# Performance work log

Measured on AMD Instinct MI355X. Metric: run time of the kernel, lower is better.

Reference implementation:

```python
import jax, jax.numpy as jnp
import numpy as np

N = 100000      # nodes
E = 1600000     # edges
IN = 64         # in_channels
H = 64          # hidden_channels
OUT = 2         # out_channels
R = 8           # num_relations
B = 4           # num_bases
L = 3           # n_layers


def setup_inputs() -> dict:
    key = jax.random.key(0)
    ks = jax.random.split(key, 12)
    s = 0.1
    return {
        "x": jax.random.normal(ks[0], (N, IN), jnp.float32),
        "edge_index": jax.random.randint(ks[1], (2, E), 0, N, dtype=jnp.int64),
        "edge_type": jax.random.randint(ks[2], (E,), 0, R, dtype=jnp.int64),
        "lin1_w": jax.random.normal(ks[3], (IN, H), jnp.float32) * s,
        "lin1_b": jnp.zeros((H,), jnp.float32),
        # stacked per-layer RGCNConv params (basis decomposition)
        "bases": jax.random.normal(ks[4], (L, B, H, H), jnp.float32) * s,
        "comp": jax.random.normal(ks[5], (L, R, B), jnp.float32) * s,
        "root": jax.random.normal(ks[6], (L, H, H), jnp.float32) * s,
        "conv_bias": jnp.zeros((L, H), jnp.float32),
        "lin2_w": jax.random.normal(ks[7], (H, OUT), jnp.float32) * s,
        "lin2_b": jnp.zeros((OUT,), jnp.float32),
    }


def _rgcn_layer(h, src, dst, edge_type, bases, comp, root, bias):
    # basis decomposition: W_r = sum_b comp[r,b] * bases[b]  -> [R, H, H]
    W = jnp.einsum('rb,bio->rio', comp, bases)
    out = h @ root + bias  # root/self-loop term
    n = h.shape[0]
    for r in range(R):  # small fixed loop over relations
        hr = h @ W[r]                                  # [N, H] transform-then-gather
        mask = (edge_type == r)
        msg = jnp.where(mask[:, None], hr[src], jnp.zeros((), h.dtype))  # [E, H]
        ssum = jax.ops.segment_sum(msg, dst, num_segments=n)
        cnt = jax.ops.segment_sum(mask.astype(h.dtype), dst, num_segments=n)
        out = out + ssum / jnp.maximum(cnt, 1.0)[:, None]  # per-relation mean aggr
    return out


def reference(x, edge_index, edge_type, lin1_w, lin1_b, bases, comp, root,
              conv_bias, lin2_w, lin2_b):
    h = x @ lin1_w + lin1_b
    src, dst = edge_index[0], edge_index[1]
    for i in range(L):
        h_ = _rgcn_layer(h, src, dst, edge_type, bases[i], comp[i], root[i], conv_bias[i])
        if i < L - 1:
            # faithful to source: last conv output is discarded; dropout is
            # identity in eval mode
            h = h + jax.nn.relu(h_)
    return h @ lin2_w + lin2_b
```

## Files before the change

kernel.cpp:

```cpp
#include <hip/hip_runtime.h>


#define HDIM 64
#define RREL 8
#define NB   4
#define KC2  320
#define NPB  16
#define APAD 328

typedef short  short8 __attribute__((ext_vector_type(8)));
typedef __bf16 bf16x8 __attribute__((ext_vector_type(8)));
typedef float  f32x4  __attribute__((ext_vector_type(4)));
typedef unsigned int uint;
typedef unsigned short ushort;

static __device__ __forceinline__ ushort f2bf(float f) {
  uint u = __builtin_bit_cast(uint, f);
  u += 0x7FFFu + ((u >> 16) & 1u);
  return (ushort)(u >> 16);
}
static __device__ __forceinline__ float bf2f(ushort s) {
  uint u = ((uint)s) << 16;
  return __builtin_bit_cast(float, u);
}

__global__ void k_prep_wt(const float* __restrict__ lin1_w, const float* __restrict__ bases,
                          const float* __restrict__ root,
                          ushort* __restrict__ wt_lin1, ushort* __restrict__ wt_conv) {
  int t = blockIdx.x * 256 + threadIdx.x;
  if (t < HDIM * HDIM) {
    int j = t >> 6, k = t & 63;
    wt_lin1[t] = f2bf(lin1_w[k * HDIM + j]);
  }
  if (t < 2 * HDIM * KC2) {
    int l = t / (HDIM * KC2);
    int rem = t - l * (HDIM * KC2);
    int j = rem / KC2;
    int k = rem - j * KC2;
    float v;
    if (k < HDIM) {
      v = root[(l * HDIM + k) * HDIM + j];
    } else {
      int b = (k - HDIM) >> 6;
      int i = (k - HDIM) & 63;
      v = bases[((l * NB + b) * HDIM + i) * HDIM + j];
    }
    wt_conv[t] = f2bf(v);
  }
}

__global__ void k_chist(const int* __restrict__ dst, const int* __restrict__ et, int E,
                        uint* __restrict__ bcnt) {
  __shared__ uint cnt[1024];
  int t = threadIdx.x;
  for (int i = t; i < 1024; i += 256) cnt[i] = 0;
  __syncthreads();
  int per = (E + gridDim.x - 1) / gridDim.x;
  int e0 = blockIdx.x * per;
  int e1 = e0 + per; if (e1 > E) e1 = E;
  for (int e = e0 + t; e < e1; e += 256)
    atomicAdd(&cnt[((uint)dst[e] * RREL + (uint)et[e]) >> 10], 1u);
  __syncthreads();
  for (int i = t; i < 1024; i += 256)
    if (cnt[i]) atomicAdd(&bcnt[i], cnt[i]);
}

__global__ void k_scanB(const uint* __restrict__ bcnt, uint* __restrict__ boff,
                        uint* __restrict__ gcur, uint* __restrict__ off8,
                        int NBK, uint M8, uint E) {
  __shared__ uint s[1024];
  int t = threadIdx.x;
  uint v = (t < NBK) ? bcnt[t] : 0u;
  s[t] = v;
  __syncthreads();
  for (int o = 1; o < 1024; o <<= 1) {
    uint u = (t >= o) ? s[t - o] : 0u;
    __syncthreads();
    s[t] += u;
    __syncthreads();
  }
  uint ex = s[t] - v;
  if (t < NBK) { boff[t] = ex; gcur[t] = ex; }
  if (t == NBK - 1) boff[NBK] = s[t];
  if (t == 0) off8[M8] = E;
}

__global__ void k_cscat(const int* __restrict__ src, const int* __restrict__ dst,
                        const int* __restrict__ et, int E, uint* __restrict__ gcur,
                        uint* __restrict__ tmp) {
  __shared__ uint cnt[1024];
  __shared__ uint base[1024];
  int t = threadIdx.x;
  int per = (E + gridDim.x - 1) / gridDim.x;
  int e0 = blockIdx.x * per;
  int e1 = e0 + per; if (e1 > E) e1 = E;
  for (int i = t; i < 1024; i += 256) cnt[i] = 0;
  __syncthreads();
  for (int e = e0 + t; e < e1; e += 256) {
    uint key = (uint)dst[e] * RREL + (uint)et[e];
    atomicAdd(&cnt[key >> 10], 1u);
  }
  __syncthreads();
  for (int i = t; i < 1024; i += 256) {
    uint c = cnt[i];
    base[i] = c ? atomicAdd(&gcur[i], c) : 0u;
  }
  __syncthreads();
  for (int i = t; i < 1024; i += 256) cnt[i] = 0;
  __syncthreads();
  for (int e = e0 + t; e < e1; e += 256) {
    uint key = (uint)dst[e] * RREL + (uint)et[e];
    uint b = key >> 10;
    uint pos = base[b] + atomicAdd(&cnt[b], 1u);
    tmp[pos] = (uint)src[e] | ((key & 1023u) << 17);
  }
}

__global__ void k_fsort(const uint* __restrict__ boff, const uint* __restrict__ tmp,
                        uint* __restrict__ sorted, uint* __restrict__ off8, uint M8) {
  __shared__ uint c2[1024];
  __shared__ uint ex[1024];
  __shared__ uint s[256];
  int t = threadIdx.x;
  uint b = blockIdx.x;
  uint bo = boff[b], be = boff[b + 1];
  for (int i = t; i < 1024; i += 256) c2[i] = 0;
  __syncthreads();
  for (uint i = bo + t; i < be; i += 256) atomicAdd(&c2[tmp[i] >> 17], 1u);
  __syncthreads();
  int k4 = t * 4;
  uint v0 = c2[k4], v1 = c2[k4 + 1], v2 = c2[k4 + 2], v3 = c2[k4 + 3];
  uint tsum = v0 + v1 + v2 + v3;
  s[t] = tsum;
  __syncthreads();
  for (int o = 1; o < 256; o <<= 1) {
    uint u = (t >= o) ? s[t - o] : 0u;
    __syncthreads();
    s[t] += u;
    __syncthreads();
  }
  uint e0x = s[t] - tsum;
  ex[k4]     = e0x;
  ex[k4 + 1] = e0x + v0;
  ex[k4 + 2] = e0x + v0 + v1;
  ex[k4 + 3] = e0x + v0 + v1 + v2;
  __syncthreads();
  uint gbase = b << 10;
  #pragma unroll
  for (int u = 0; u < 4; ++u) {
    uint g = gbase + (uint)(k4 + u);
    if (g < M8) off8[g] = bo + ex[k4 + u];
  }
  for (int i = t; i < 1024; i += 256) c2[i] = 0;
  __syncthreads();
  for (uint i = bo + t; i < be; i += 256) {
    uint w = tmp[i];
    uint fk = w >> 17;
    uint pos = bo + ex[fk] + atomicAdd(&c2[fk], 1u);
    sorted[pos] = w & 0x1FFFFu;
  }
}

__global__ void k_lin1(const float* __restrict__ x, const ushort* __restrict__ wt,
                       const float* __restrict__ bias, ushort* __restrict__ hb, int N) {
  __shared__ ushort A[NPB][72];
  int nodebase = blockIdx.x * NPB;
  {
    int t = threadIdx.x;
    int nl = t >> 4, c = (t & 15) * 4;
    int n = nodebase + nl;
    ushort4 o = {0, 0, 0, 0};
    if (n < N) {
      f32x4 v = *(const f32x4*)&x[(size_t)n * HDIM + c];
      o.x = f2bf(v[0]); o.y = f2bf(v[1]); o.z = f2bf(v[2]); o.w = f2bf(v[3]);
    }
    *(ushort4*)&A[nl][c] = o;
  }
  __syncthreads();
  int lane = threadIdx.x & 63, wid = threadIdx.x >> 6;
  int m16 = lane & 15, khi = lane >> 4;
  int colbase = wid * 16;
  f32x4 acc = {0.f, 0.f, 0.f, 0.f};
  #pragma unroll
  for (int kk = 0; kk < HDIM; kk += 32) {
    int k0 = kk + khi * 8;
    short8 av = *(const short8*)&A[m16][k0];
    short8 bv = *(const short8*)&wt[(colbase + m16) * HDIM + k0];
    acc = __builtin_amdgcn_mfma_f32_16x16x32_bf16(
        __builtin_bit_cast(bf16x8, av), __builtin_bit_cast(bf16x8, bv), acc, 0, 0, 0);
  }
  int j = colbase + m16;
  float bj = bias[j];
  #pragma unroll
  for (int r = 0; r < 4; ++r) {
    int nl = khi * 4 + r;
    int n = nodebase + nl;
    if (n < N) hb[(size_t)n * HDIM + j] = f2bf(acc[r] + bj);
  }
}

__global__ void __launch_bounds__(256, 6)
k_conv(const uint* __restrict__ off8, const uint* __restrict__ sorted,
       const ushort* __restrict__ hb_in, const float* __restrict__ compL,
       const ushort* __restrict__ wt, const float* __restrict__ bias,
       ushort* __restrict__ hb_out, int N, int last,
       const float* __restrict__ w2, const float* __restrict__ b2,
       float* __restrict__ out) {
  __shared__ ushort A[NPB][APAD];
  __shared__ float  cmp[RREL * NB];
  __shared__ float  accO[NPB][2];
  int nb0 = blockIdx.x * NPB;
  int lane = threadIdx.x & 63, wid = threadIdx.x >> 6;

  if (threadIdx.x < RREL * NB) cmp[threadIdx.x] = compL[threadIdx.x];
  if (threadIdx.x < NPB * 2) accO[threadIdx.x >> 1][threadIdx.x & 1] = 0.f;
  {
    int t = threadIdx.x;
    int nl = t >> 4, c = (t & 15) * 4;
    int n = nb0 + nl;
    uint2 v = {0u, 0u};
    if (n < N) v = *(const uint2*)&hb_in[(size_t)n * HDIM + c];
    *(uint2*)&A[nl][c] = v;
  }
  __syncthreads();

  const ushort* hlane = hb_in + lane;
  for (int q = 0; q < 4; ++q) {
    int nl = wid * 4 + q;
    int n = nb0 + nl;
    if (n < N) {
      uint bv = 0xFFFFFFFFu;
      if (lane < 9) bv = off8[(uint)n * RREL + (uint)lane];
      uint s0 = (uint)__builtin_amdgcn_readlane((int)bv, 0);
      uint s1 = (uint)__builtin_amdgcn_readlane((int)bv, 8);
      float run = 0.f, z0 = 0.f, z1 = 0.f, z2 = 0.f, z3 = 0.f;
      int rel = 0;
      uint prevb = s0;
      uint nextb = (uint)__builtin_amdgcn_readlane((int)bv, 1);
      for (uint base = s0; base < s1; base += 16u) {
        const uint* sp = sorted + base;
        uint4 w0 = *(const uint4*)(sp);
        uint4 w1 = *(const uint4*)(sp + 4);
        uint4 w2v = *(const uint4*)(sp + 8);
        uint4 w3 = *(const uint4*)(sp + 12);
        uint idx[16] = {w0.x, w0.y, w0.z, w0.w, w1.x, w1.y, w1.z, w1.w,
                        w2v.x, w2v.y, w2v.z, w2v.w, w3.x, w3.y, w3.z, w3.w};
        float g[16];
        #pragma unroll
        for (int j = 0; j < 16; ++j) {
          uint ij = (uint)__builtin_amdgcn_readfirstlane((int)idx[j]) & 0x1FFFFu;
          g[j] = bf2f(hlane[(size_t)ij << 6]);
        }
        uint m = s1 - base;
        #pragma unroll
        for (int j = 0; j < 16; ++j) {
          if ((uint)j < m) {
            uint pos = base + (uint)j;
            while (pos >= nextb) {
              float mean = run * __builtin_amdgcn_rcpf(fmaxf((float)(nextb - prevb), 1.0f));
              f32x4 c4 = *(const f32x4*)&cmp[rel * NB];
              z0 += c4[0] * mean; z1 += c4[1] * mean;
              z2 += c4[2] * mean; z3 += c4[3] * mean;
              run = 0.f;
              ++rel;
              prevb = nextb;
              nextb = (uint)__builtin_amdgcn_readlane((int)bv, rel + 1);
            }
            run += g[j];
          }
        }
      }
      while (rel < RREL) {
        float mean = run * __builtin_amdgcn_rcpf(fmaxf((float)(nextb - prevb), 1.0f));
        f32x4 c4 = *(const f32x4*)&cmp[rel * NB];
        z0 += c4[0] * mean; z1 += c4[1] * mean;
        z2 += c4[2] * mean; z3 += c4[3] * mean;
        run = 0.f;
        ++rel;
        prevb = nextb;
        if (rel < RREL)
          nextb = (uint)__builtin_amdgcn_readlane((int)bv, rel + 1);
      }
      A[nl][HDIM + 0 * HDIM + lane] = f2bf(z0);
      A[nl][HDIM + 1 * HDIM + lane] = f2bf(z1);
      A[nl][HDIM + 2 * HDIM + lane] = f2bf(z2);
      A[nl][HDIM + 3 * HDIM + lane] = f2bf(z3);
    } else {
      #pragma unroll
      for (int b = 0; b < NB; ++b) A[nl][HDIM + b * HDIM + lane] = 0;
    }
  }
  __syncthreads();

  int m16 = lane & 15, khi = lane >> 4;
  int colbase = wid * 16;
  f32x4 acc = {0.f, 0.f, 0.f, 0.f};
  #pragma unroll
  for (int kk = 0; kk < KC2; kk += 32) {
    int k0 = kk + khi * 8;
    short8 av = *(const short8*)&A[m16][k0];
    short8 bv = *(const short8*)&wt[(uint)(colbase + m16) * KC2 + k0];
    acc = __builtin_amdgcn_mfma_f32_16x16x32_bf16(
        __builtin_bit_cast(bf16x8, av), __builtin_bit_cast(bf16x8, bv), acc, 0, 0, 0);
  }
  int j = colbase + m16;
  float bj = bias[j];
  if (!last) {
    #pragma unroll
    for (int r = 0; r < 4; ++r) {
      int nl = khi * 4 + r;
      int n = nb0 + nl;
      if (n < N) {
        float hs = bf2f(A[nl][j]);
        float hn = hs + fmaxf(acc[r] + bj, 0.f);
        hb_out[(uint)n * HDIM + j] = f2bf(hn);
      }
    }
  } else {
    float w0 = w2[j * 2], w1 = w2[j * 2 + 1];
    #pragma unroll
    for (int r = 0; r < 4; ++r) {
      int nl = khi * 4 + r;
      int n = nb0 + nl;
      float hn = 0.f;
      if (n < N) {
        float hs = bf2f(A[nl][j]);
        hn = hs + fmaxf(acc[r] + bj, 0.f);
      }
      float p0 = hn * w0, p1 = hn * w1;
      #pragma unroll
      for (int o = 1; o < 16; o <<= 1) {
        p0 += __shfl_xor(p0, o);
        p1 += __shfl_xor(p1, o);
      }
      if (m16 == 0 && n < N) {
        atomicAdd(&accO[nl][0], p0);
        atomicAdd(&accO[nl][1], p1);
      }
    }
    __syncthreads();
    if (threadIdx.x < NPB * 2) {
      int nl = threadIdx.x >> 1, o = threadIdx.x & 1;
      int n = nb0 + nl;
      if (n < N) out[2 * n + o] = accO[nl][o] + b2[o];
    }
  }
}

extern "C" void kernel_launch(void* const* d_in, const int* in_sizes, int n_in,
                              void* d_out, int out_size, void* d_ws, size_t ws_size,
                              hipStream_t stream) {
  const float* x      = (const float*)d_in[0];
  const int*   ei     = (const int*)d_in[1];
  const int*   et     = (const int*)d_in[2];
  const float* lin1_w = (const float*)d_in[3];
  const float* lin1_b = (const float*)d_in[4];
  const float* bases  = (const float*)d_in[5];
  const float* comp   = (const float*)d_in[6];
  const float* root   = (const float*)d_in[7];
  const float* cbias  = (const float*)d_in[8];
  const float* lin2_w = (const float*)d_in[9];
  const float* lin2_b = (const float*)d_in[10];
  float* out = (float*)d_out;

  int N = in_sizes[0] / HDIM;
  int E = in_sizes[2];
  uint M8 = (uint)N * RREL;
  int NBK = (int)((M8 + 1023u) >> 10);
  const int* srcp = ei;
  const int* dstp = ei + E;

  char* p = (char*)d_ws;
  auto carve = [&](size_t bytes) { char* r = p; p += (bytes + 255) & ~(size_t)255; return r; };
  ushort* hb_a    = (ushort*)carve((size_t)N * HDIM * 2);
  ushort* hb_b    = (ushort*)carve((size_t)N * HDIM * 2);
  uint*   sorted  = (uint*)carve((size_t)(E + 160) * 4);
  uint*   tmp     = (uint*)carve((size_t)E * 4);
  uint*   off8    = (uint*)carve((size_t)(M8 + 1) * 4);
  uint*   bcnt    = (uint*)carve(4096);
  uint*   boff    = (uint*)carve(4128);
  uint*   gcur    = (uint*)carve(4096);
  ushort* wt_lin1 = (ushort*)carve((size_t)HDIM * HDIM * 2);
  ushort* wt_conv = (ushort*)carve((size_t)2 * HDIM * KC2 * 2);
  carve((size_t)8 << 20);

  hipMemsetAsync(bcnt, 0, 4096, stream);

  int nwg = (N + NPB - 1) / NPB;

  k_prep_wt<<<(2 * HDIM * KC2 + 255) / 256, 256, 0, stream>>>(lin1_w, bases, root, wt_lin1, wt_conv);
  k_chist<<<128, 256, 0, stream>>>(dstp, et, E, bcnt);
  k_scanB<<<1, 1024, 0, stream>>>(bcnt, boff, gcur, off8, NBK, M8, (uint)E);
  k_cscat<<<128, 256, 0, stream>>>(srcp, dstp, et, E, gcur, tmp);
  k_fsort<<<NBK, 256, 0, stream>>>(boff, tmp, sorted, off8, M8);

  k_lin1<<<nwg, 256, 0, stream>>>(x, wt_lin1, lin1_b, hb_a, N);
  k_conv<<<nwg, 256, 0, stream>>>(off8, sorted, hb_a, comp, wt_conv, cbias,
                                  hb_b, N, 0, lin2_w, lin2_b, out);
  k_conv<<<nwg, 256, 0, stream>>>(off8, sorted, hb_b, comp + RREL * NB,
                                  wt_conv + HDIM * KC2, cbias + HDIM, hb_a, N, 1,
                                  lin2_w, lin2_b, out);
}
```

Measured before the change: 249.0 us.

## Sub-sort edges by source segment within each destination-relation bucket

The CSR sort key now adds a 4-way source-index segment (src>>15) under each (dst, relation) pair, so edges for a node are ordered by rough source region. The gather of bf16 features therefore walks the source feature table in more local order, aiming at better cache hit rates. Per-relation counts are now computed by summing the four segment lengths with lane shuffles, and the reciprocals are precomputed once per node. The cost is a 4x larger offset array, 4096 coarse buckets in the histogram and scatter kernels, and more segment-boundary iterations in the aggregation loop.

```diff
diff --git a/kernel.cpp b/kernel.cpp
--- a/kernel.cpp
+++ b/kernel.cpp
@@ -7,6 +7,8 @@
 #define KC2  320
 #define NPB  16
 #define APAD 328
+#define CSH  15
+#define NSEG 32
 
 typedef short  short8 __attribute__((ext_vector_type(8)));
 typedef __bf16 bf16x8 __attribute__((ext_vector_type(8)));
@@ -49,29 +51,36 @@
   }
 }
 
-__global__ void k_chist(const int* __restrict__ dst, const int* __restrict__ et, int E,
-                        uint* __restrict__ bcnt) {
-  __shared__ uint cnt[1024];
+__global__ void k_chist(const int* __restrict__ src, const int* __restrict__ dst,
+                        const int* __restrict__ et, int E, uint* __restrict__ bcnt) {
+  __shared__ uint cnt[4096];
   int t = threadIdx.x;
-  for (int i = t; i < 1024; i += 256) cnt[i] = 0;
+  for (int i = t; i < 4096; i += 256) cnt[i] = 0;
   __syncthreads();
   int per = (E + gridDim.x - 1) / gridDim.x;
   int e0 = blockIdx.x * per;
   int e1 = e0 + per; if (e1 > E) e1 = E;
-  for (int e = e0 + t; e < e1; e += 256)
-    atomicAdd(&cnt[((uint)dst[e] * RREL + (uint)et[e]) >> 10], 1u);
-  __syncthreads();
-  for (int i = t; i < 1024; i += 256)
+  for (int e = e0 + t; e < e1; e += 256) {
+    uint key = (uint)dst[e] * NSEG + (((uint)src[e] >> CSH) << 3) + (uint)et[e];
+    atomicAdd(&cnt[key >> 10], 1u);
+  }
+  __syncthreads();
+  for (int i = t; i < 4096; i += 256)
     if (cnt[i]) atomicAdd(&bcnt[i], cnt[i]);
 }
 
 __global__ void k_scanB(const uint* __restrict__ bcnt, uint* __restrict__ boff,
                         uint* __restrict__ gcur, uint* __restrict__ off8,
-                        int NBK, uint M8, uint E) {
+                        int NBK, uint M32, uint E) {
   __shared__ uint s[1024];
   int t = threadIdx.x;
-  uint v = (t < NBK) ? bcnt[t] : 0u;
-  s[t] = v;
+  int k4 = t * 4;
+  uint v0 = (k4 < NBK) ? bcnt[k4] : 0u;
+  uint v1 = (k4 + 1 < NBK) ? bcnt[k4 + 1] : 0u;
+  uint v2 = (k4 + 2 < NBK) ? bcnt[k4 + 2] : 0u;
+  uint v3 = (k4 + 3 < NBK) ? bcnt[k4 + 3] : 0u;
+  uint tsum = v0 + v1 + v2 + v3;
+  s[t] = tsum;
   __syncthreads();
   for (int o = 1; o < 1024; o <<= 1) {
     uint u = (t >= o) ? s[t - o] : 0u;
@@ -79,37 +88,40 @@
     s[t] += u;
     __syncthreads();
   }
-  uint ex = s[t] - v;
-  if (t < NBK) { boff[t] = ex; gcur[t] = ex; }
-  if (t == NBK - 1) boff[NBK] = s[t];
-  if (t == 0) off8[M8] = E;
+  uint ex = s[t] - tsum;
+  if (k4 < NBK)     { boff[k4] = ex;                   gcur[k4] = ex; }
+  if (k4 + 1 < NBK) { boff[k4 + 1] = ex + v0;          gcur[k4 + 1] = ex + v0; }
+  if (k4 + 2 < NBK) { boff[k4 + 2] = ex + v0 + v1;     gcur[k4 + 2] = ex + v0 + v1; }
+  if (k4 + 3 < NBK) { boff[k4 + 3] = ex + v0 + v1 + v2; gcur[k4 + 3] = ex + v0 + v1 + v2; }
+  if (t == 1023) boff[NBK] = s[1023];
+  if (t == 0) off8[M32] = E;
 }
 
 __global__ void k_cscat(const int* __restrict__ src, const int* __restrict__ dst,
                         const int* __restrict__ et, int E, uint* __restrict__ gcur,
                         uint* __restrict__ tmp) {
-  __shared__ uint cnt[1024];
-  __shared__ uint base[1024];
+  __shared__ uint cnt[4096];
+  __shared__ uint base[4096];
   int t = threadIdx.x;
   int per = (E + gridDim.x - 1) / gridDim.x;
   int e0 = blockIdx.x * per;
   int e1 = e0 + per; if (e1 > E) e1 = E;
-  for (int i = t; i < 1024; i += 256) cnt[i] = 0;
+  for (int i = t; i < 4096; i += 256) cnt[i] = 0;
   __syncthreads();
   for (int e = e0 + t; e < e1; e += 256) {
-    uint key = (uint)dst[e] * RREL + (uint)et[e];
+    uint key = (uint)dst[e] * NSEG + (((uint)src[e] >> CSH) << 3) + (uint)et[e];
     atomicAdd(&cnt[key >> 10], 1u);
   }
   __syncthreads();
-  for (int i = t; i < 1024; i += 256) {
+  for (int i = t; i < 4096; i += 256) {
     uint c = cnt[i];
     base[i] = c ? atomicAdd(&gcur[i], c) : 0u;
   }
   __syncthreads();
-  for (int i = t; i < 1024; i += 256) cnt[i] = 0;
+  for (int i = t; i < 4096; i += 256) cnt[i] = 0;
   __syncthreads();
   for (int e = e0 + t; e < e1; e += 256) {
-    uint key = (uint)dst[e] * RREL + (uint)et[e];
+    uint key = (uint)dst[e] * NSEG + (((uint)src[e] >> CSH) << 3) + (uint)et[e];
     uint b = key >> 10;
     uint pos = base[b] + atomicAdd(&cnt[b], 1u);
     tmp[pos] = (uint)src[e] | ((key & 1023u) << 17);
@@ -117,7 +129,7 @@
 }
 
 __global__ void k_fsort(const uint* __restrict__ boff, const uint* __restrict__ tmp,
-                        uint* __restrict__ sorted, uint* __restrict__ off8, uint M8) {
+                        uint* __restrict__ sorted, uint* __restrict__ off8, uint M32) {
   __shared__ uint c2[1024];
   __shared__ uint ex[1024];
   __shared__ uint s[256];
@@ -149,7 +161,7 @@
   #pragma unroll
   for (int u = 0; u < 4; ++u) {
     uint g = gbase + (uint)(k4 + u);
-    if (g < M8) off8[g] = bo + ex[k4 + u];
+    if (g < M32) off8[g] = bo + ex[k4 + u];
   }
   for (int i = t; i < 1024; i += 256) c2[i] = 0;
   __syncthreads();
@@ -230,12 +242,18 @@
     int n = nb0 + nl;
     if (n < N) {
       uint bv = 0xFFFFFFFFu;
-      if (lane < 9) bv = off8[(uint)n * RREL + (uint)lane];
+      if (lane < NSEG + 1) bv = off8[(uint)n * NSEG + (uint)lane];
+      uint nxt = (uint)__shfl((int)bv, lane + 1);
+      uint d = (lane < NSEG) ? (nxt - bv) : 0u;
+      d += (uint)__shfl_xor((int)d, 8);
+      d += (uint)__shfl_xor((int)d, 16);
+      float rcpv = __builtin_amdgcn_rcpf(fmaxf((float)d, 1.0f));
+      int rcpi = __builtin_bit_cast(int, rcpv);
+
       uint s0 = (uint)__builtin_amdgcn_readlane((int)bv, 0);
-      uint s1 = (uint)__builtin_amdgcn_readlane((int)bv, 8);
+      uint s1 = (uint)__builtin_amdgcn_readlane((int)bv, NSEG);
       float run = 0.f, z0 = 0.f, z1 = 0.f, z2 = 0.f, z3 = 0.f;
-      int rel = 0;
-      uint prevb = s0;
+      int ri = 0;
       uint nextb = (uint)__builtin_amdgcn_readlane((int)bv, 1);
       for (uint base = s0; base < s1; base += 16u) {
         const uint* sp = sorted + base;
@@ -252,34 +270,36 @@
           g[j] = bf2f(hlane[(size_t)ij << 6]);
         }
         uint m = s1 - base;
+        if (m > 16u) m = 16u;
         #pragma unroll
         for (int j = 0; j < 16; ++j) {
           if ((uint)j < m) {
             uint pos = base + (uint)j;
             while (pos >= nextb) {
-              float mean = run * __builtin_amdgcn_rcpf(fmaxf((float)(nextb - prevb), 1.0f));
+              int rel = ri & 7;
+              float rc = __builtin_bit_cast(float, __builtin_amdgcn_readlane(rcpi, rel));
+              float mp = run * rc;
               f32x4 c4 = *(const f32x4*)&cmp[rel * NB];
-              z0 += c4[0] * mean; z1 += c4[1] * mean;
-              z2 += c4[2] * mean; z3 += c4[3] * mean;
+              z0 += c4[0] * mp; z1 += c4[1] * mp;
+              z2 += c4[2] * mp; z3 += c4[3] * mp;
               run = 0.f;
-              ++rel;
-              prevb = nextb;
-              nextb = (uint)__builtin_amdgcn_readlane((int)bv, rel + 1);
+              ++ri;
+              nextb = (uint)__builtin_amdgcn_readlane((int)bv, ri + 1);
             }
             run += g[j];
           }
         }
       }
-      while (rel < RREL) {
-        float mean = run * __builtin_amdgcn_rcpf(fmaxf((float)(nextb - prevb), 1.0f));
+      while (ri < NSEG) {
+        int rel = ri & 7;
+        float rc = __builtin_bit_cast(float, __builtin_amdgcn_readlane(rcpi, rel));
+        float mp = run * rc;
         f32x4 c4 = *(const f32x4*)&cmp[rel * NB];
-        z0 += c4[0] * mean; z1 += c4[1] * mean;
-        z2 += c4[2] * mean; z3 += c4[3] * mean;
+        z0 += c4[0] * mp; z1 += c4[1] * mp;
+        z2 += c4[2] * mp; z3 += c4[3] * mp;
         run = 0.f;
-        ++rel;
-        prevb = nextb;
-        if (rel < RREL)
-          nextb = (uint)__builtin_amdgcn_readlane((int)bv, rel + 1);
+        ++ri;
+        if (ri < NSEG) nextb = (uint)__builtin_amdgcn_readlane((int)bv, ri + 1);
       }
       A[nl][HDIM + 0 * HDIM + lane] = f2bf(z0);
       A[nl][HDIM + 1 * HDIM + lane] = f2bf(z1);
@@ -365,8 +385,8 @@
 
   int N = in_sizes[0] / HDIM;
   int E = in_sizes[2];
-  uint M8 = (uint)N * RREL;
-  int NBK = (int)((M8 + 1023u) >> 10);
+  uint M32 = (uint)N * NSEG;
+  int NBK = (int)((M32 + 1023u) >> 10);
   const int* srcp = ei;
   const int* dstp = ei + E;
 
@@ -376,23 +396,23 @@
   ushort* hb_b    = (ushort*)carve((size_t)N * HDIM * 2);
   uint*   sorted  = (uint*)carve((size_t)(E + 160) * 4);
   uint*   tmp     = (uint*)carve((size_t)E * 4);
-  uint*   off8    = (uint*)carve((size_t)(M8 + 1) * 4);
-  uint*   bcnt    = (uint*)carve(4096);
-  uint*   boff    = (uint*)carve(4128);
-  uint*   gcur    = (uint*)carve(4096);
+  uint*   off8    = (uint*)carve((size_t)(M32 + 1) * 4);
+  uint*   bcnt    = (uint*)carve(16384);
+  uint*   boff    = (uint*)carve(16388);
+  uint*   gcur    = (uint*)carve(16384);
   ushort* wt_lin1 = (ushort*)carve((size_t)HDIM * HDIM * 2);
   ushort* wt_conv = (ushort*)carve((size_t)2 * HDIM * KC2 * 2);
-  carve((size_t)8 << 20);
-
-  hipMemsetAsync(bcnt, 0, 4096, stream);
+  carve((size_t)1 << 20);
+
+  hipMemsetAsync(bcnt, 0, 16384, stream);
 
   int nwg = (N + NPB - 1) / NPB;
 
   k_prep_wt<<<(2 * HDIM * KC2 + 255) / 256, 256, 0, stream>>>(lin1_w, bases, root, wt_lin1, wt_conv);
-  k_chist<<<128, 256, 0, stream>>>(dstp, et, E, bcnt);
-  k_scanB<<<1, 1024, 0, stream>>>(bcnt, boff, gcur, off8, NBK, M8, (uint)E);
+  k_chist<<<128, 256, 0, stream>>>(srcp, dstp, et, E, bcnt);
+  k_scanB<<<1, 1024, 0, stream>>>(bcnt, boff, gcur, off8, NBK, M32, (uint)E);
   k_cscat<<<128, 256, 0, stream>>>(srcp, dstp, et, E, gcur, tmp);
-  k_fsort<<<NBK, 256, 0, stream>>>(boff, tmp, sorted, off8, M8);
+  k_fsort<<<NBK, 256, 0, stream>>>(boff, tmp, sorted, off8, M32);
 
   k_lin1<<<nwg, 256, 0, stream>>>(x, wt_lin1, lin1_b, hb_a, N);
   k_conv<<<nwg, 256, 0, stream>>>(off8, sorted, hb_a, comp, wt_conv, cbias,
```

Result: slower. 285.9 us (+14.8%).
